# Kernel optimization log

Hardware: AMD Instinct MI355X
Metric: run time of the kernel (lower is better)

## Reference

```python
import jax, jax.numpy as jnp
import numpy as np

H = 256
I = 32
O = 10


def setup_inputs() -> dict:
    key = jax.random.key(0)
    ks = jax.random.split(key, 16)
    stdv = 1.0 / np.sqrt(H)
    u = lambda k, shape: jax.random.uniform(k, shape, jnp.float32, -stdv, stdv)
    x = jax.random.normal(ks[0], (256, 512, I), jnp.float32)
    return {
        "x": x,
        "Wgx": u(ks[1], (I, H)), "Wgh": u(ks[2], (H, H)), "bg": u(ks[3], (H,)),
        "Wix": u(ks[4], (I, H)), "Wih": u(ks[5], (H, H)), "bi": u(ks[6], (H,)),
        "Wfx": u(ks[7], (I, H)), "Wfh": u(ks[8], (H, H)), "bf": u(ks[9], (H,)),
        "Wox": u(ks[10], (I, H)), "Woh": u(ks[11], (H, H)), "bo": u(ks[12], (H,)),
        "Wph": u(ks[13], (H, O)), "bp": u(ks[14], (O,)),
    }


def _lstm_forward(x, Wgx, Wgh, bg, Wix, Wih, bi, Wfx, Wfh, bf, Wox, Woh, bo, Wph, bp):
    B, S, _ = x.shape
    # Precompute all input projections in one big GEMM: (B,S,I) @ (I,4H) -> (B,S,4H)
    Wx = jnp.concatenate([Wgx, Wix, Wfx, Wox], axis=1)      # (I, 4H)
    bx = jnp.concatenate([bg, bi, bf, bo], axis=0)          # (4H,)
    xproj = jnp.einsum("bsi,ik->bsk", x, Wx) + bx           # (B, S, 4H)
    Wh = jnp.concatenate([Wgh, Wih, Wfh, Woh], axis=1)      # (H, 4H)

    # Note: torch code skips the h@Wh term at t=0; with h0=c0=0 the math is identical.
    def step(carry, xp_t):
        h, c = carry
        z = xp_t + h @ Wh                                   # (B, 4H)
        g = jnp.tanh(z[:, 0 * H:1 * H])
        i = jax.nn.sigmoid(z[:, 1 * H:2 * H])
        f = jax.nn.sigmoid(z[:, 2 * H:3 * H])
        o = jax.nn.sigmoid(z[:, 3 * H:4 * H])
        c = g * i + c * f
        h = jnp.tanh(c) * o
        return (h, c), None

    h0 = jnp.zeros((B, H), x.dtype)
    c0 = jnp.zeros((B, H), x.dtype)
    (h, _), _ = jax.lax.scan(step, (h0, c0), jnp.swapaxes(xproj, 0, 1))
    out = h @ Wph + bp                                      # (B, O)
    return jax.nn.softmax(out, axis=1)


def reference(x, Wgx, Wgh, bg, Wix, Wih, bi, Wfx, Wfh, bf, Wox, Woh, bo, Wph, bp):
    return _lstm_forward(x, Wgx, Wgh, bg, Wix, Wih, bi, Wfx, Wfh, bf, Wox, Woh, bo, Wph, bp)
```

## Files before the change

kernel.cpp:

```cpp
#include <hip/hip_runtime.h>

#define HD 256
#define ID 32
#define OD 10
#define SEQ 512
#define NBG 16
#define FLAGS_OFF 589824
#define HX_OFF    622592
#define SMEM_BYTES (16384 + 65536)

typedef __attribute__((ext_vector_type(4))) float f32x4;
typedef __attribute__((ext_vector_type(8))) unsigned short u16x8;
typedef __attribute__((ext_vector_type(8))) __bf16 bf16x8;
struct U2 { unsigned long long a, b; };

static __device__ __forceinline__ unsigned short f2bf(float f) {
  unsigned u = __builtin_bit_cast(unsigned, f);
  u += 0x7fffu + ((u >> 16) & 1u);
  return (unsigned short)(u >> 16);
}
static __device__ __forceinline__ float bf2f(unsigned short s) {
  unsigned u = ((unsigned)s) << 16;
  return __builtin_bit_cast(float, u);
}
static __device__ __forceinline__ f32x4 mfma16(u16x8 a, u16x8 b, f32x4 c) {
  return __builtin_amdgcn_mfma_f32_16x16x32_bf16(
      __builtin_bit_cast(bf16x8, a), __builtin_bit_cast(bf16x8, b), c, 0, 0, 0);
}
static __device__ __forceinline__ float fast_sigmoid(float x) {
  return 1.f / (1.f + __expf(-x));
}
static __device__ __forceinline__ float fast_tanh(float x) {
  return 1.f - 2.f / (__expf(2.f * x) + 1.f);
}

__global__ void pack_w(const float* __restrict__ Wgx, const float* __restrict__ Wgh,
                       const float* __restrict__ Wix, const float* __restrict__ Wih,
                       const float* __restrict__ Wfx, const float* __restrict__ Wfh,
                       const float* __restrict__ Wox, const float* __restrict__ Woh,
                       unsigned short* __restrict__ Wpk) {
  int p = blockIdx.x * blockDim.x + threadIdx.x;
  if (p >= 576 * 64) return;
  int f = p >> 6, l = p & 63;
  int hw = f / 36, r = f % 36;
  int g = r / 9, kt = r % 9;
  int U = hw * 16 + (l & 15);
  const float* Wx[4] = {Wgx, Wix, Wfx, Wox};
  const float* Wh[4] = {Wgh, Wih, Wfh, Woh};
  u16x8 v;
  #pragma unroll
  for (int i = 0; i < 8; ++i) {
    int k = kt * 32 + 8 * (l >> 4) + i;
    float val = (k < ID) ? Wx[g][k * HD + U] : Wh[g][(k - ID) * HD + U];
    v[i] = f2bf(val);
  }
  *(u16x8*)(Wpk + ((size_t)f << 9) + (l << 3)) = v;
}

template <int HF>
static __device__ __forceinline__ void mfma_own(
    const u16x8 (&wf)[4][7], const unsigned short* wlds_w, int l,
    const u16x8& ax, const u16x8 (&aown)[4], f32x4 (&acc)[4], bool full) {
  #pragma unroll
  for (int g = 0; g < 4; ++g) acc[g] = mfma16(ax, wf[g][0], acc[g]);
  if (!full) return;
  #pragma unroll
  for (int k2 = 0; k2 < 4; ++k2) {
    const int kt = 1 + 4 * HF + k2;
    #pragma unroll
    for (int g = 0; g < 4; ++g) {
      u16x8 bw;
      if (kt <= 6) bw = wf[g][kt];
      else bw = *(const u16x8*)(wlds_w + (g * 2 + (kt - 7)) * 512 + l * 8);
      acc[g] = mfma16(aown[k2], bw, acc[g]);
    }
  }
}
template <int HF>
static __device__ __forceinline__ void mfma_part(
    const u16x8 (&wf)[4][7], const unsigned short* wlds_w, int l,
    const u16x8 (&apart)[4], f32x4 (&acc)[4]) {
  #pragma unroll
  for (int k2 = 0; k2 < 4; ++k2) {
    const int kt = 1 + 4 * (1 - HF) + k2;
    #pragma unroll
    for (int g = 0; g < 4; ++g) {
      u16x8 bw;
      if (kt <= 6) bw = wf[g][kt];
      else bw = *(const u16x8*)(wlds_w + (g * 2 + (kt - 7)) * 512 + l * 8);
      acc[g] = mfma16(apart[k2], bw, acc[g]);
    }
  }
}

__global__ void __launch_bounds__(512, 2) lstm_rec(
    const float* __restrict__ x, const unsigned short* __restrict__ Wpk,
    const float* __restrict__ bgp, const float* __restrict__ bip,
    const float* __restrict__ bfp, const float* __restrict__ bop,
    const float* __restrict__ Wph, const float* __restrict__ bpp,
    unsigned int* __restrict__ flags, void* __restrict__ hx,
    float* __restrict__ out) {
  extern __shared__ __align__(16) char smem[];
  unsigned short* hbuf = (unsigned short*)smem;
  unsigned short* wlds = (unsigned short*)(smem + 16384);

  const int tid = threadIdx.x;
  const int w = tid >> 6, l = tid & 63;
  const int l15 = l & 15, l4 = l >> 4;
  const int bgi = blockIdx.x & 15, hf = blockIdx.x >> 4;
  const int b0 = bgi * 16;
  char* hxc = (char*)hx;
  unsigned int* myflag = flags + bgi * 2 + hf;
  unsigned int* pflag  = flags + bgi * 2 + (1 - hf);

  const unsigned short* wbase =
      Wpk + (((size_t)(hf * 8 + w) * 36) << 9) + (l << 3);
  unsigned short* wlds_w = wlds + w * 4096;

  #pragma unroll
  for (int g = 0; g < 4; ++g)
    #pragma unroll
    for (int d = 0; d < 2; ++d) {
      u16x8 v = *(const u16x8*)(wbase + ((size_t)(g * 9 + 7 + d) << 9));
      *(u16x8*)(wlds_w + (g * 2 + d) * 512 + l * 8) = v;
    }
  u16x8 wf[4][7];
  #pragma unroll
  for (int g = 0; g < 4; ++g)
    #pragma unroll
    for (int kt = 0; kt < 7; ++kt)
      wf[g][kt] = *(const u16x8*)(wbase + ((size_t)(g * 9 + kt) << 9));

  float bias[4];
  {
    const float* bs[4] = {bgp, bip, bfp, bop};
    #pragma unroll
    for (int g = 0; g < 4; ++g) bias[g] = bs[g][hf * 128 + w * 16 + l15];
  }
  float cst[4] = {0.f, 0.f, 0.f, 0.f};

  const float* xrow = x + ((size_t)(b0 + l15) * SEQ) * ID + 8 * l4;
  float4 xv0 = *(const float4*)xrow;
  float4 xv1 = *(const float4*)(xrow + 4);

  __syncthreads();

  #pragma unroll 1
  for (int t = 0; t < SEQ; ++t) {
    u16x8 ax;
    ax[0] = f2bf(xv0.x); ax[1] = f2bf(xv0.y); ax[2] = f2bf(xv0.z); ax[3] = f2bf(xv0.w);
    ax[4] = f2bf(xv1.x); ax[5] = f2bf(xv1.y); ax[6] = f2bf(xv1.z); ax[7] = f2bf(xv1.w);
    {
      int tn = (t + 1 < SEQ) ? (t + 1) : t;
      xv0 = *(const float4*)(xrow + (size_t)tn * ID);
      xv1 = *(const float4*)(xrow + (size_t)tn * ID + 4);
    }

    const int pr = (t - 1) & 1;
    u16x8 aown[4];
    if (t > 0) {
      const unsigned short* hb = hbuf + pr * 4096 + l15 * 256;
      #pragma unroll
      for (int k2 = 0; k2 < 4; ++k2) {
        int c = 4 * (4 * hf + k2) + l4;
        aown[k2] = *(const u16x8*)(hb + ((c ^ l15) & 31) * 8);
      }
      if (w == 0) {
        while (__hip_atomic_load(pflag, __ATOMIC_ACQUIRE,
                                 __HIP_MEMORY_SCOPE_AGENT) < (unsigned)t) {}
        const unsigned long long* pp = (const unsigned long long*)
            (hxc + (size_t)((pr * NBG + bgi) * 2 + (1 - hf)) * 4096) + l * 8;
        unsigned long long d0[8];
        #pragma unroll
        for (int q = 0; q < 8; ++q)
          d0[q] = __hip_atomic_load(pp + q, __ATOMIC_RELAXED,
                                    __HIP_MEMORY_SCOPE_AGENT);
        int r = l >> 2;
        unsigned short* hw_ = hbuf + pr * 4096 + r * 256;
        #pragma unroll
        for (int q = 0; q < 4; ++q) {
          int gu = (1 - hf) * 128 + (l & 3) * 32 + q * 8;
          int ch = (gu >> 3) ^ r;
          U2 u{d0[2 * q], d0[2 * q + 1]};
          *(u16x8*)(hw_ + ch * 8) = __builtin_bit_cast(u16x8, u);
        }
      }
    }

    f32x4 acc[4];
    #pragma unroll
    for (int g = 0; g < 4; ++g)
      acc[g] = f32x4{bias[g], bias[g], bias[g], bias[g]};
    if (hf == 0) mfma_own<0>(wf, wlds_w, l, ax, aown, acc, t > 0);
    else         mfma_own<1>(wf, wlds_w, l, ax, aown, acc, t > 0);

    __syncthreads();

    if (t > 0) {
      u16x8 apart[4];
      const unsigned short* hb = hbuf + pr * 4096 + l15 * 256;
      #pragma unroll
      for (int k2 = 0; k2 < 4; ++k2) {
        int c = 4 * (4 * (1 - hf) + k2) + l4;
        apart[k2] = *(const u16x8*)(hb + ((c ^ l15) & 31) * 8);
      }
      if (hf == 0) mfma_part<0>(wf, wlds_w, l, apart, acc);
      else         mfma_part<1>(wf, wlds_w, l, apart, acc);
    }

    unsigned short* ho = hbuf + (t & 1) * 4096;
    unsigned int* hxo = (unsigned int*)
        (hxc + (size_t)(((t & 1) * NBG + bgi) * 2 + hf) * 4096);
    int ul = 16 * w + l15;
    #pragma unroll
    for (int i = 0; i < 4; ++i) {
      float gg = fast_tanh(acc[0][i]);
      float ii = fast_sigmoid(acc[1][i]);
      float ff = fast_sigmoid(acc[2][i]);
      float oo = fast_sigmoid(acc[3][i]);
      float cc = gg * ii + cst[i] * ff;
      cst[i] = cc;
      float hh = fast_tanh(cc) * oo;
      unsigned short me = f2bf(hh);
      int r = 4 * l4 + i;
      int gu = hf * 128 + ul;
      ho[r * 256 + (((gu >> 3) ^ r) & 31) * 8 + (gu & 7)] = me;
      unsigned int ov = __shfl_xor((unsigned int)me, 1, 64);
      if ((l & 1) == 0) {
        unsigned int packed = (unsigned int)me | (ov << 16);
        __hip_atomic_store(hxo + r * 64 + (ul >> 1), packed,
                           __ATOMIC_RELAXED, __HIP_MEMORY_SCOPE_AGENT);
      }
    }
    __syncthreads();
    if (tid == 0)
      __hip_atomic_store(myflag, (unsigned)(t + 1), __ATOMIC_RELEASE,
                         __HIP_MEMORY_SCOPE_AGENT);
  }

  if (hf == 0) {
    if (w == 0) {
      while (__hip_atomic_load(pflag, __ATOMIC_ACQUIRE,
                               __HIP_MEMORY_SCOPE_AGENT) < (unsigned)SEQ) {}
      const unsigned long long* pp = (const unsigned long long*)
          (hxc + (size_t)((1 * NBG + bgi) * 2 + 1) * 4096) + l * 8;
      unsigned long long d0[8];
      #pragma unroll
      for (int q = 0; q < 8; ++q)
        d0[q] = __hip_atomic_load(pp + q, __ATOMIC_RELAXED,
                                  __HIP_MEMORY_SCOPE_AGENT);
      int r = l >> 2;
      unsigned short* hw_ = hbuf + 4096 + r * 256;
      #pragma unroll
      for (int q = 0; q < 4; ++q) {
        int gu = 128 + (l & 3) * 32 + q * 8;
        int ch = (gu >> 3) ^ r;
        U2 u{d0[2 * q], d0[2 * q + 1]};
        *(u16x8*)(hw_ + ch * 8) = __builtin_bit_cast(u16x8, u);
      }
    }
    __syncthreads();
    float* lbuf = (float*)(smem + 16384);
    if (tid < 16 * OD) {
      int eb = tid & 15, ej = tid >> 4;
      float s = bpp[ej];
      for (int k = 0; k < HD; ++k)
        s += bf2f(hbuf[4096 + eb * 256 + (((k >> 3) ^ eb) & 31) * 8 + (k & 7)]) *
             Wph[k * OD + ej];
      lbuf[eb * OD + ej] = s;
    }
    __syncthreads();
    if (tid < 16) {
      float m = -1e30f;
      #pragma unroll
      for (int j = 0; j < OD; ++j) m = fmaxf(m, lbuf[tid * OD + j]);
      float e[OD], sum = 0.f;
      #pragma unroll
      for (int j = 0; j < OD; ++j) { e[j] = __expf(lbuf[tid * OD + j] - m); sum += e[j]; }
      float inv = 1.f / sum;
      #pragma unroll
      for (int j = 0; j < OD; ++j) out[(b0 + tid) * OD + j] = e[j] * inv;
    }
  }
}

extern "C" void kernel_launch(void* const* d_in, const int* in_sizes, int n_in,
                              void* d_out, int out_size, void* d_ws, size_t ws_size,
                              hipStream_t stream) {
  const float* X   = (const float*)d_in[0];
  const float* Wgx = (const float*)d_in[1];
  const float* Wgh = (const float*)d_in[2];
  const float* bg  = (const float*)d_in[3];
  const float* Wix = (const float*)d_in[4];
  const float* Wih = (const float*)d_in[5];
  const float* bi  = (const float*)d_in[6];
  const float* Wfx = (const float*)d_in[7];
  const float* Wfh = (const float*)d_in[8];
  const float* bf  = (const float*)d_in[9];
  const float* Wox = (const float*)d_in[10];
  const float* Woh = (const float*)d_in[11];
  const float* bo  = (const float*)d_in[12];
  const float* Wph = (const float*)d_in[13];
  const float* bp  = (const float*)d_in[14];

  unsigned short* Wpk   = (unsigned short*)d_ws;
  unsigned int*   flags = (unsigned int*)((char*)d_ws + FLAGS_OFF);
  void*           hx    = (char*)d_ws + HX_OFF;

  hipMemsetAsync((char*)d_ws + FLAGS_OFF, 0, 32 * 4, stream);
  (void)hipFuncSetAttribute((const void*)lstm_rec,
                            hipFuncAttributeMaxDynamicSharedMemorySize,
                            SMEM_BYTES);

  pack_w<<<dim3(72), dim3(512), 0, stream>>>(Wgx, Wgh, Wix, Wih, Wfx, Wfh,
                                             Wox, Woh, Wpk);
  lstm_rec<<<dim3(32), dim3(512), SMEM_BYTES, stream>>>(
      X, Wpk, bg, bi, bf, bo, Wph, bp, flags, hx, (float*)d_out);
}
```

Before: 1.821 ms.

## Have every wave read partner hidden state directly and drop mid-step barrier

Each wave now polls the partner block's flag itself with a relaxed load and an acquire fence, then loads its partner h fragments straight from global memory into registers. This removes the wave-0 copy into LDS and the __syncthreads that sat between the own-half and partner-half MFMAs. The h export now writes full rows in coalesced 8-byte stores after an LDS staging barrier, instead of shuffle-packed atomic stores. Flags are padded to 128 bytes each to avoid false sharing. The cost is more global polling traffic from all waves and an extra barrier in the publish path.

```diff
diff --git a/kernel.cpp b/kernel.cpp
--- a/kernel.cpp
+++ b/kernel.cpp
@@ -12,7 +12,6 @@
 typedef __attribute__((ext_vector_type(4))) float f32x4;
 typedef __attribute__((ext_vector_type(8))) unsigned short u16x8;
 typedef __attribute__((ext_vector_type(8))) __bf16 bf16x8;
-struct U2 { unsigned long long a, b; };
 
 static __device__ __forceinline__ unsigned short f2bf(float f) {
   unsigned u = __builtin_bit_cast(unsigned, f);
@@ -110,8 +109,8 @@
   const int bgi = blockIdx.x & 15, hf = blockIdx.x >> 4;
   const int b0 = bgi * 16;
   char* hxc = (char*)hx;
-  unsigned int* myflag = flags + bgi * 2 + hf;
-  unsigned int* pflag  = flags + bgi * 2 + (1 - hf);
+  unsigned int* myflag = flags + (bgi * 2 + hf) * 32;
+  unsigned int* pflag  = flags + (bgi * 2 + (1 - hf)) * 32;
 
   const unsigned short* wbase =
       Wpk + (((size_t)(hf * 8 + w) * 36) << 9) + (l << 3);
@@ -142,6 +141,10 @@
   const float* xrow = x + ((size_t)(b0 + l15) * SEQ) * ID + 8 * l4;
   float4 xv0 = *(const float4*)xrow;
   float4 xv1 = *(const float4*)(xrow + 4);
+
+  const int ro = tid >> 5, u0 = (tid & 31) * 4;
+  const int pgu = hf * 128 + u0;
+  const int pofs = ro * 256 + ((((pgu >> 3) ^ ro) & 31) * 8) + (pgu & 7);
 
   __syncthreads();
 
@@ -157,34 +160,22 @@
     }
 
     const int pr = (t - 1) & 1;
-    u16x8 aown[4];
+    u16x8 aown[4], apart[4];
     if (t > 0) {
+      while (__hip_atomic_load(pflag, __ATOMIC_RELAXED,
+                               __HIP_MEMORY_SCOPE_AGENT) < (unsigned)t) {}
+      __builtin_amdgcn_fence(__ATOMIC_ACQUIRE, "agent");
+      const unsigned short* pp = (const unsigned short*)
+          (hxc + (size_t)((pr * NBG + bgi) * 2 + (1 - hf)) * 4096) + l15 * 128;
+      #pragma unroll
+      for (int k2 = 0; k2 < 4; ++k2)
+        apart[k2] = *(const u16x8*)(pp + 32 * k2 + 8 * l4);
       const unsigned short* hb = hbuf + pr * 4096 + l15 * 256;
       #pragma unroll
       for (int k2 = 0; k2 < 4; ++k2) {
         int c = 4 * (4 * hf + k2) + l4;
         aown[k2] = *(const u16x8*)(hb + ((c ^ l15) & 31) * 8);
       }
-      if (w == 0) {
-        while (__hip_atomic_load(pflag, __ATOMIC_ACQUIRE,
-                                 __HIP_MEMORY_SCOPE_AGENT) < (unsigned)t) {}
-        const unsigned long long* pp = (const unsigned long long*)
-            (hxc + (size_t)((pr * NBG + bgi) * 2 + (1 - hf)) * 4096) + l * 8;
-        unsigned long long d0[8];
-        #pragma unroll
-        for (int q = 0; q < 8; ++q)
-          d0[q] = __hip_atomic_load(pp + q, __ATOMIC_RELAXED,
-                                    __HIP_MEMORY_SCOPE_AGENT);
-        int r = l >> 2;
-        unsigned short* hw_ = hbuf + pr * 4096 + r * 256;
-        #pragma unroll
-        for (int q = 0; q < 4; ++q) {
-          int gu = (1 - hf) * 128 + (l & 3) * 32 + q * 8;
-          int ch = (gu >> 3) ^ r;
-          U2 u{d0[2 * q], d0[2 * q + 1]};
-          *(u16x8*)(hw_ + ch * 8) = __builtin_bit_cast(u16x8, u);
-        }
-      }
     }
 
     f32x4 acc[4];
@@ -193,24 +184,12 @@
       acc[g] = f32x4{bias[g], bias[g], bias[g], bias[g]};
     if (hf == 0) mfma_own<0>(wf, wlds_w, l, ax, aown, acc, t > 0);
     else         mfma_own<1>(wf, wlds_w, l, ax, aown, acc, t > 0);
-
-    __syncthreads();
-
     if (t > 0) {
-      u16x8 apart[4];
-      const unsigned short* hb = hbuf + pr * 4096 + l15 * 256;
-      #pragma unroll
-      for (int k2 = 0; k2 < 4; ++k2) {
-        int c = 4 * (4 * (1 - hf) + k2) + l4;
-        apart[k2] = *(const u16x8*)(hb + ((c ^ l15) & 31) * 8);
-      }
       if (hf == 0) mfma_part<0>(wf, wlds_w, l, apart, acc);
       else         mfma_part<1>(wf, wlds_w, l, apart, acc);
     }
 
     unsigned short* ho = hbuf + (t & 1) * 4096;
-    unsigned int* hxo = (unsigned int*)
-        (hxc + (size_t)(((t & 1) * NBG + bgi) * 2 + hf) * 4096);
     int ul = 16 * w + l15;
     #pragma unroll
     for (int i = 0; i < 4; ++i) {
@@ -221,16 +200,17 @@
       float cc = gg * ii + cst[i] * ff;
       cst[i] = cc;
       float hh = fast_tanh(cc) * oo;
-      unsigned short me = f2bf(hh);
       int r = 4 * l4 + i;
       int gu = hf * 128 + ul;
-      ho[r * 256 + (((gu >> 3) ^ r) & 31) * 8 + (gu & 7)] = me;
-      unsigned int ov = __shfl_xor((unsigned int)me, 1, 64);
-      if ((l & 1) == 0) {
-        unsigned int packed = (unsigned int)me | (ov << 16);
-        __hip_atomic_store(hxo + r * 64 + (ul >> 1), packed,
-                           __ATOMIC_RELAXED, __HIP_MEMORY_SCOPE_AGENT);
-      }
+      ho[r * 256 + (((gu >> 3) ^ r) & 31) * 8 + (gu & 7)] = f2bf(hh);
+    }
+    __syncthreads();
+
+    {
+      unsigned long long v = *(const unsigned long long*)(ho + pofs);
+      unsigned long long* dst = (unsigned long long*)
+          (hxc + (size_t)(((t & 1) * NBG + bgi) * 2 + hf) * 4096);
+      dst[(ro * 128 + u0) >> 2] = v;
     }
     __syncthreads();
     if (tid == 0)
@@ -240,23 +220,17 @@
 
   if (hf == 0) {
     if (w == 0) {
-      while (__hip_atomic_load(pflag, __ATOMIC_ACQUIRE,
+      while (__hip_atomic_load(pflag, __ATOMIC_RELAXED,
                                __HIP_MEMORY_SCOPE_AGENT) < (unsigned)SEQ) {}
-      const unsigned long long* pp = (const unsigned long long*)
-          (hxc + (size_t)((1 * NBG + bgi) * 2 + 1) * 4096) + l * 8;
-      unsigned long long d0[8];
-      #pragma unroll
-      for (int q = 0; q < 8; ++q)
-        d0[q] = __hip_atomic_load(pp + q, __ATOMIC_RELAXED,
-                                  __HIP_MEMORY_SCOPE_AGENT);
-      int r = l >> 2;
-      unsigned short* hw_ = hbuf + 4096 + r * 256;
+      __builtin_amdgcn_fence(__ATOMIC_ACQUIRE, "agent");
+      const unsigned short* pp = (const unsigned short*)
+          (hxc + (size_t)((1 * NBG + bgi) * 2 + 1) * 4096);
+      int er = l >> 2, eu0 = (l & 3) * 32;
       #pragma unroll
       for (int q = 0; q < 4; ++q) {
-        int gu = 128 + (l & 3) * 32 + q * 8;
-        int ch = (gu >> 3) ^ r;
-        U2 u{d0[2 * q], d0[2 * q + 1]};
-        *(u16x8*)(hw_ + ch * 8) = __builtin_bit_cast(u16x8, u);
+        u16x8 v = *(const u16x8*)(pp + er * 128 + eu0 + 8 * q);
+        int gu = 128 + eu0 + 8 * q;
+        *(u16x8*)(hbuf + 4096 + er * 256 + (((gu >> 3) ^ er) & 31) * 8) = v;
       }
     }
     __syncthreads();
@@ -307,7 +281,7 @@
   unsigned int*   flags = (unsigned int*)((char*)d_ws + FLAGS_OFF);
   void*           hx    = (char*)d_ws + HX_OFF;
 
-  hipMemsetAsync((char*)d_ws + FLAGS_OFF, 0, 32 * 4, stream);
+  hipMemsetAsync((char*)d_ws + FLAGS_OFF, 0, 32 * 32 * 4, stream);
   (void)hipFuncSetAttribute((const void*)lstm_rec,
                             hipFuncAttributeMaxDynamicSharedMemorySize,
                             SMEM_BYTES);
```

After: 2.204 ms. 1.21x slower.
